# Performance work log

Measured on AMD Instinct MI355X. Metric: run time of the kernel, lower is better.

Reference implementation:

```python
import jax, jax.numpy as jnp
import numpy as np

B, M, N, C, D, H, TOPK = 32, 20000, 500000, 128, 128, 4, 100
EPS = 1e-5


def setup_inputs() -> dict:
    key = jax.random.key(0)
    ks = jax.random.split(key, 24)
    f = lambda k, s: jax.random.normal(k, s, dtype=jnp.float32) * 0.05
    inp = {
        'lhs_embedding': f(ks[0], (B, C)),
        'rhs_gnn_embedding': f(ks[1], (M, C)),
        'rhs_emb_weight': f(ks[2], (N, D)),
        'proj_W': f(ks[3], (D, C)), 'proj_b': jnp.zeros((D,), jnp.float32),
        'head_W': f(ks[4], (1, C)), 'head_b': jnp.zeros((1,), jnp.float32),
        'off_emb_W': f(ks[5], (1, D)), 'off_emb_b': jnp.zeros((1,), jnp.float32),
        'off_id_W': f(ks[6], (1, D)), 'off_id_b': jnp.zeros((1,), jnp.float32),
        'Wq': f(ks[7], (D, D)), 'bq': jnp.zeros((D,), jnp.float32),
        'Wk': f(ks[8], (D, D)), 'bk': jnp.zeros((D,), jnp.float32),
        'Wv': f(ks[9], (D, D)), 'bv': jnp.zeros((D,), jnp.float32),
        'Wo': f(ks[10], (D, D)), 'bo': jnp.zeros((D,), jnp.float32),
        'ln1_g': jnp.ones((D,), jnp.float32), 'ln1_b': jnp.zeros((D,), jnp.float32),
        'ffn_W': f(ks[11], (D, D)), 'ffn_b': jnp.zeros((D,), jnp.float32),
        'ln2_g': jnp.ones((D,), jnp.float32), 'ln2_b': jnp.zeros((D,), jnp.float32),
        'rhs_idgnn_index': jax.random.randint(ks[12], (M,), 0, N, dtype=jnp.int32),
        'lhs_idgnn_batch': jnp.sort(jax.random.randint(ks[13], (M,), 0, B, dtype=jnp.int32)),
    }
    return inp


def _ln(x, g, b):
    mu = jnp.mean(x, axis=-1, keepdims=True)
    var = jnp.mean(jnp.square(x - mu), axis=-1, keepdims=True)
    return (x - mu) * jax.lax.rsqrt(var + EPS) * g + b


def reference(lhs_embedding, rhs_gnn_embedding, rhs_emb_weight, proj_W, proj_b,
              head_W, head_b, off_emb_W, off_emb_b, off_id_W, off_id_b,
              Wq, bq, Wk, bk, Wv, bv, Wo, bo, ln1_g, ln1_b, ffn_W, ffn_b,
              ln2_g, ln2_b, rhs_idgnn_index, lhs_idgnn_batch):
    # --- embgnn logits: dense [B,N] matmul + per-row offset ---
    lhs_proj = lhs_embedding @ proj_W.T + proj_b                          # [B,D]
    embgnn_logits = lhs_proj @ rhs_emb_weight.T                           # [B,N]
    embgnn_logits = embgnn_logits + (lhs_proj @ off_emb_W[0] + off_emb_b[0])[:, None]

    # --- idgnn logits on sampled rhs nodes ---
    idgnn_logits = rhs_gnn_embedding @ head_W[0] + head_b[0]              # [M]
    idgnn_logits = idgnn_logits + jnp.sum(lhs_embedding[lhs_idgnn_batch] * rhs_gnn_embedding, axis=-1)
    idgnn_offset = lhs_proj @ off_id_W[0] + off_id_b[0]                   # [B]
    idgnn_logits = idgnn_logits + idgnn_offset[lhs_idgnn_batch]

    # scatter idgnn logits into the dense logits tensor
    embgnn_logits = embgnn_logits.at[lhs_idgnn_batch, rhs_idgnn_index].set(idgnn_logits)

    # --- final rhs embeddings: shallow table + scattered GNN embeddings ---
    copy_tensor = jnp.zeros_like(rhs_emb_weight).at[rhs_idgnn_index].set(rhs_gnn_embedding)
    final_rhs_embed = rhs_emb_weight + copy_tensor                        # [N,D]

    # --- rerank: topk -> gather -> MAB -> scatter back ---
    _, topk_index = jax.lax.top_k(embgnn_logits, TOPK)                    # [B,TOPK]
    top_embed = final_rhs_embed[topk_index]                               # [B,TOPK,D]

    dh = D // H
    q = (top_embed @ Wq.T + bq).reshape(B, TOPK, H, dh)
    k = (top_embed @ Wk.T + bk).reshape(B, TOPK, H, dh)
    v = (top_embed @ Wv.T + bv).reshape(B, TOPK, H, dh)
    att = jnp.einsum('bthd,bshd->bhts', q, k) / jnp.sqrt(jnp.float32(dh))
    att = jax.nn.softmax(att, axis=-1)
    o = jnp.einsum('bhts,bshd->bthd', att, v).reshape(B, TOPK, D) @ Wo.T + bo
    x = _ln(top_embed + o, ln1_g, ln1_b)
    x = _ln(x + jax.nn.relu(x @ ffn_W.T + ffn_b), ln2_g, ln2_b)           # tr_embed [B,TOPK,D]

    # original code passes lhs_proj[lhs_idgnn_batch] and indexes rows 0..B-1
    lhs_q = lhs_proj[lhs_idgnn_batch][:B]                                 # [B,D]
    scores = jnp.sum(lhs_q[:, None, :] * x, axis=-1)                      # [B,TOPK]
    rows = jnp.arange(B)[:, None]
    transformer_logits = jnp.full((B, N), -jnp.inf, dtype=embgnn_logits.dtype)
    transformer_logits = transformer_logits.at[rows, topk_index].set(scores)

    return embgnn_logits, transformer_logits, topk_index
```

## Files before the change

kernel.cpp:

```cpp
#include <hip/hip_runtime.h>

typedef unsigned long long u64;
typedef unsigned int u32;

#define N_NODES 500000
#define M_SAMP  20000
#define BB      32
#define DD      128
#define TOPK    100
#define NBINS   2048
#define CAP     2048
#define C4PB    3907
#define LN_EPS  1e-5f
#define NEG_BIG -1.0e30f

__device__ __forceinline__ u32 fkey(float x) {
  u32 u = __float_as_uint(x);
  u32 mask = (u32)((int)u >> 31) | 0x80000000u;
  return u ^ mask;
}

__global__ __launch_bounds__(256) void k_front(
    const float* __restrict__ lhs, const float* __restrict__ pW,
    const float* __restrict__ pb, const float* __restrict__ oeW,
    const float* __restrict__ oeb, const float* __restrict__ oiW,
    const float* __restrict__ oib, const float* __restrict__ rgnn,
    const float* __restrict__ hW, const float* __restrict__ hb,
    const int* __restrict__ ridx, const int* __restrict__ rbat,
    float* __restrict__ lhs_proj, float* __restrict__ lhs_projT,
    float* __restrict__ oe_sc, float* __restrict__ oi_sc,
    float* __restrict__ val, int* __restrict__ win,
    int* __restrict__ inv, u32* __restrict__ hist, u32* __restrict__ cand_cnt) {
  int bid = blockIdx.x, tid = threadIdx.x;
  if (bid < 32) {
    __shared__ float lrow[DD];
    __shared__ float red[DD];
    int b = bid, d = tid;
    if (d < DD) lrow[d] = lhs[b * DD + d];
    __syncthreads();
    float acc = 0.f;
    if (d < DD) {
      acc = pb[d];
      for (int c = 0; c < DD; ++c) acc += lrow[c] * pW[d * DD + c];
      lhs_proj[b * DD + d] = acc;
      lhs_projT[d * BB + b] = acc;
      red[d] = acc * oeW[d];
    }
    __syncthreads();
    for (int s = 64; s > 0; s >>= 1) { if (d < s) red[d] += red[d + s]; __syncthreads(); }
    if (d == 0) oe_sc[b] = red[0] + oeb[0];
    __syncthreads();
    if (d < DD) red[d] = acc * oiW[d];
    __syncthreads();
    for (int s = 64; s > 0; s >>= 1) { if (d < s) red[d] += red[d + s]; __syncthreads(); }
    if (d == 0) oi_sc[b] = red[0] + oib[0];
  } else if (bid < 32 + M_SAMP / 4) {
    int wid = tid >> 6, lane = tid & 63;
    int m = (bid - 32) * 4 + wid;
    if (m >= M_SAMP) return;
    int b = rbat[m], n = ridx[m];
    float2 rg = ((const float2*)(rgnn + (size_t)m * DD))[lane];
    float2 hw = ((const float2*)hW)[lane];
    float2 le = ((const float2*)(lhs + (size_t)b * DD))[lane];
    float p = rg.x * hw.x + rg.y * hw.y + rg.x * le.x + rg.y * le.y;
    for (int off = 32; off > 0; off >>= 1) p += __shfl_down(p, off);
    int w = 1;
    for (int j0 = m + 1; j0 < M_SAMP; j0 += 64) {
      int j = j0 + lane;
      bool inb = (j < M_SAMP) && (rbat[j] == b);
      bool match = inb && (ridx[j] == n);
      if (__ballot(match)) { w = 0; break; }
      if (__ballot(inb) != ~0ULL) break;
    }
    if (lane == 0) { val[m] = p + hb[0]; win[m] = w; }
  } else {
    int i = (bid - (32 + M_SAMP / 4)) * 256 + tid;
    if (i < N_NODES) inv[i] = -1;
    if (i < BB * NBINS) hist[i] = 0;
    if (i < BB) cand_cnt[i] = 0;
  }
}

__global__ __launch_bounds__(256) void k_embgnn(const float* __restrict__ rhs,
    const float* __restrict__ lhsT, const float* __restrict__ oe_sc,
    float* __restrict__ out, float* __restrict__ tr) {
  __shared__ float sT[64][DD + 4];
  int tid = threadIdx.x;
  long n0 = (long)blockIdx.x * 64;
  #pragma unroll
  for (int p = 0; p < 8; ++p) {
    int f = p * 256 + tid;
    int r = f >> 5, c4 = (f & 31) << 2;
    long n = n0 + r; if (n >= N_NODES) n = N_NODES - 1;
    float4 v = *(const float4*)(rhs + n * DD + c4);
    sT[r][c4] = v.x; sT[r][c4 + 1] = v.y; sT[r][c4 + 2] = v.z; sT[r][c4 + 3] = v.w;
  }
  __syncthreads();
  int lane = tid & 63;
  int bg = __builtin_amdgcn_readfirstlane((tid >> 6) * 8);
  float acc[8];
  #pragma unroll
  for (int j = 0; j < 8; ++j) acc[j] = 0.f;
  const float4* srow = (const float4*)&sT[lane][0];
  #pragma unroll 4
  for (int cq = 0; cq < 32; ++cq) {
    float4 rv = srow[cq];
    const float* lp = lhsT + cq * 4 * BB + bg;
    #pragma unroll
    for (int j = 0; j < 8; ++j) {
      acc[j] += lp[j] * rv.x;
      acc[j] += lp[BB + j] * rv.y;
      acc[j] += lp[2 * BB + j] * rv.z;
      acc[j] += lp[3 * BB + j] * rv.w;
    }
  }
  long n = n0 + lane;
  if (n < N_NODES) {
    #pragma unroll
    for (int j = 0; j < 8; ++j) {
      out[(long)(bg + j) * N_NODES + n] = acc[j] + oe_sc[bg + j];
      tr[(long)(bg + j) * N_NODES + n] = NEG_BIG;
    }
  }
}

__global__ void k_scatter2(const int* __restrict__ ridx, const int* __restrict__ rbat,
                           const float* __restrict__ val, const int* __restrict__ win,
                           const float* __restrict__ oi_sc,
                           int* __restrict__ inv, float* __restrict__ out) {
  int m = blockIdx.x * 256 + threadIdx.x;
  if (m < M_SAMP) {
    atomicMax(&inv[ridx[m]], m);
    if (win[m]) {
      int b = rbat[m];
      out[(long)b * N_NODES + ridx[m]] = val[m] + oi_sc[b];
    }
  }
}

__global__ void k_hist(const float* __restrict__ out, u32* __restrict__ hist) {
  __shared__ u32 hsh[NBINS];
  int tid = threadIdx.x;
  for (int i = tid; i < NBINS; i += 256) hsh[i] = 0;
  __syncthreads();
  int row = blockIdx.y;
  const float4* o4 = (const float4*)out + (long)row * (N_NODES / 4);
  int start = blockIdx.x * C4PB;
  int end = min(start + C4PB, N_NODES / 4);
  for (int i = start + tid; i < end; i += 256) {
    float4 v = o4[i];
    atomicAdd(&hsh[fkey(v.x) >> 21], 1u);
    atomicAdd(&hsh[fkey(v.y) >> 21], 1u);
    atomicAdd(&hsh[fkey(v.z) >> 21], 1u);
    atomicAdd(&hsh[fkey(v.w) >> 21], 1u);
  }
  __syncthreads();
  for (int i = tid; i < NBINS; i += 256)
    if (hsh[i]) atomicAdd(&hist[row * NBINS + i], hsh[i]);
}

__global__ void k_collect(const float* __restrict__ out, const u32* __restrict__ hist,
                          u32* __restrict__ cand_cnt, u64* __restrict__ cand) {
  __shared__ u32 part[256];
  __shared__ int s_cb;
  int tid = threadIdx.x, row = blockIdx.y;
  const u32* hrow = hist + row * NBINS;
  u32 p = 0;
  #pragma unroll
  for (int j = 0; j < 8; ++j) p += hrow[tid * 8 + j];
  part[tid] = p;
  __syncthreads();
  if (tid == 0) {
    u32 cum = 0; int g = 255, found = 0;
    for (; g > 0; --g) { cum += part[g]; if (cum >= TOPK) { found = 1; break; } }
    u32 c2 = found ? (cum - part[g]) : cum;
    int hi = found ? g * 8 + 7 : 7;
    int bin;
    for (bin = hi; bin > 0; --bin) { c2 += hrow[bin]; if (c2 >= TOPK) break; }
    s_cb = bin;
  }
  __syncthreads();
  u32 cb = (u32)s_cb;
  const float4* o4 = (const float4*)out + (long)row * (N_NODES / 4);
  int start = blockIdx.x * C4PB;
  int end = min(start + C4PB, N_NODES / 4);
  for (int i = start + tid; i < end; i += 256) {
    float4 v = o4[i];
    u32 kk[4] = { fkey(v.x), fkey(v.y), fkey(v.z), fkey(v.w) };
    #pragma unroll
    for (int j = 0; j < 4; ++j) {
      if ((kk[j] >> 21) >= cb) {
        u32 pos = atomicAdd(&cand_cnt[row], 1u);
        int idx = i * 4 + j;
        if (pos < CAP) cand[(long)row * CAP + pos] = ((u64)kk[j] << 32) | (u32)(~idx);
      }
    }
  }
}

__global__ __launch_bounds__(1024) void k_sort(const u64* __restrict__ cand,
                                               const u32* __restrict__ cand_cnt,
                                               int* __restrict__ topk_out) {
  __shared__ u64 sh[CAP];
  int row = blockIdx.x, tid = threadIdx.x;
  int cnt = min((int)cand_cnt[row], CAP);
  int NS = 128; while (NS < cnt) NS <<= 1;
  for (int i = tid; i < NS; i += 1024) sh[i] = (i < cnt) ? cand[(long)row * CAP + i] : 0ULL;
  __syncthreads();
  for (int k2 = 2; k2 <= NS; k2 <<= 1) {
    for (int j = k2 >> 1; j > 0; j >>= 1) {
      for (int i = tid; i < NS; i += 1024) {
        int ixj = i ^ j;
        if (ixj > i) {
          u64 a = sh[i], c = sh[ixj];
          bool up = ((i & k2) == 0);
          if (up ? (a < c) : (a > c)) { sh[i] = c; sh[ixj] = a; }
        }
      }
      __syncthreads();
    }
  }
  if (tid < TOPK) topk_out[row * TOPK + tid] = (int)(~(u32)sh[tid]);
}

__global__ __launch_bounds__(128) void k_gqkv(const int* __restrict__ topk,
    const int* __restrict__ inv, const float* __restrict__ rhs_emb,
    const float* __restrict__ rgnn,
    const float* __restrict__ Wq, const float* __restrict__ bq,
    const float* __restrict__ Wk, const float* __restrict__ bk,
    const float* __restrict__ Wv, const float* __restrict__ bv,
    float* __restrict__ q, float* __restrict__ k_, float* __restrict__ v_) {
  __shared__ float xr[16][DD];
  __shared__ int sn[16], sm[16];
  int tid = threadIdx.x;
  long r0 = (long)blockIdx.x * 16;
  if (tid < 16) { int n = topk[r0 + tid]; sn[tid] = n; sm[tid] = inv[n]; }
  __syncthreads();
  for (int i = tid; i < 16 * DD; i += 128) {
    int r = i >> 7, dd_ = i & 127;
    int n = sn[r], mw = sm[r];
    float v = rhs_emb[(long)n * DD + dd_];
    if (mw >= 0) v += rgnn[(long)mw * DD + dd_];
    xr[r][dd_] = v;
  }
  __syncthreads();
  float aq[16], ak[16], av[16];
  float bqv = bq[tid], bkv = bk[tid], bvv = bv[tid];
  #pragma unroll
  for (int r = 0; r < 16; ++r) { aq[r] = bqv; ak[r] = bkv; av[r] = bvv; }
  const float4* Wq4 = (const float4*)(Wq + tid * DD);
  const float4* Wk4 = (const float4*)(Wk + tid * DD);
  const float4* Wv4 = (const float4*)(Wv + tid * DD);
  #pragma unroll 4
  for (int c4 = 0; c4 < 32; ++c4) {
    float4 wq = Wq4[c4], wk = Wk4[c4], wv = Wv4[c4];
    #pragma unroll
    for (int r = 0; r < 16; ++r) {
      const float* xa = &xr[r][c4 << 2];
      float x0v = xa[0], x1v = xa[1], x2v = xa[2], x3v = xa[3];
      aq[r] += x0v * wq.x + x1v * wq.y + x2v * wq.z + x3v * wq.w;
      ak[r] += x0v * wk.x + x1v * wk.y + x2v * wk.z + x3v * wk.w;
      av[r] += x0v * wv.x + x1v * wv.y + x2v * wv.z + x3v * wv.w;
    }
  }
  #pragma unroll
  for (int r = 0; r < 16; ++r) {
    q[(r0 + r) * DD + tid] = aq[r];
    k_[(r0 + r) * DD + tid] = ak[r];
    v_[(r0 + r) * DD + tid] = av[r];
  }
}

__global__ __launch_bounds__(128) void k_att(const float* __restrict__ q,
    const float* __restrict__ k_, const float* __restrict__ v_, float* __restrict__ o) {
  __shared__ float kv[TOPK][32];
  __shared__ float att[TOPK][TOPK];
  int b = blockIdx.x >> 2, h = blockIdx.x & 3;
  int tid = threadIdx.x;
  long base = (long)b * TOPK * DD + h * 32;
  for (int i = tid; i < TOPK * 32; i += 128) {
    int t = i >> 5, d = i & 31;
    kv[t][d] = k_[base + (long)t * DD + d];
  }
  __syncthreads();
  int t = tid;
  if (t < TOPK) {
    float4 q4[8];
    const float4* qp = (const float4*)(q + base + (long)t * DD);
    #pragma unroll
    for (int i = 0; i < 8; ++i) q4[i] = qp[i];
    float qreg[32];
    #pragma unroll
    for (int i = 0; i < 8; ++i) {
      qreg[4 * i] = q4[i].x; qreg[4 * i + 1] = q4[i].y;
      qreg[4 * i + 2] = q4[i].z; qreg[4 * i + 3] = q4[i].w;
    }
    const float scale = 0.17677669529663687f;
    for (int s = 0; s < TOPK; ++s) {
      float sum = 0.f;
      #pragma unroll
      for (int d = 0; d < 32; ++d) sum += qreg[d] * kv[s][d];
      att[t][s] = sum * scale;
    }
    float mx = att[t][0];
    for (int s = 1; s < TOPK; ++s) mx = fmaxf(mx, att[t][s]);
    float sum = 0.f;
    for (int s = 0; s < TOPK; ++s) { float e = expf(att[t][s] - mx); att[t][s] = e; sum += e; }
    float inv = 1.f / sum;
    for (int s = 0; s < TOPK; ++s) att[t][s] *= inv;
  }
  __syncthreads();
  for (int i = tid; i < TOPK * 32; i += 128) {
    int tt = i >> 5, d = i & 31;
    kv[tt][d] = v_[base + (long)tt * DD + d];
  }
  __syncthreads();
  if (t < TOPK) {
    float osum[32];
    #pragma unroll
    for (int d = 0; d < 32; ++d) osum[d] = 0.f;
    for (int s = 0; s < TOPK; ++s) {
      float a = att[t][s];
      #pragma unroll
      for (int d = 0; d < 32; ++d) osum[d] += a * kv[s][d];
    }
    float4* op = (float4*)(o + base + (long)t * DD);
    #pragma unroll
    for (int i = 0; i < 8; ++i)
      op[i] = make_float4(osum[4 * i], osum[4 * i + 1], osum[4 * i + 2], osum[4 * i + 3]);
  }
}

__global__ __launch_bounds__(128) void k_xform(const float* __restrict__ ob_,
    const float* __restrict__ Wo, const float* __restrict__ bo,
    const int* __restrict__ topk, const int* __restrict__ inv,
    const float* __restrict__ rhs_emb, const float* __restrict__ rgnn,
    const float* __restrict__ g1, const float* __restrict__ be1,
    const float* __restrict__ fW, const float* __restrict__ fb,
    const float* __restrict__ g2, const float* __restrict__ be2,
    const float* __restrict__ lhs_proj, const int* __restrict__ lbat,
    float* __restrict__ tr) {
  __shared__ float sA[16][DD];
  __shared__ float sT[16][DD + 4];
  __shared__ float sMu[16], sRs[16];
  __shared__ int sn[16], sm[16];
  int tid = threadIdx.x;
  long r0 = (long)blockIdx.x * 16;
  if (tid < 16) { int n = topk[r0 + tid]; sn[tid] = n; sm[tid] = inv[n]; }
  for (int i = tid; i < 16 * DD; i += 128) sA[i >> 7][i & 127] = ob_[r0 * DD + i];
  __syncthreads();
  float vacc[16];
  #pragma unroll
  for (int r = 0; r < 16; ++r) vacc[r] = bo[tid];
  const float4* Wo4 = (const float4*)(Wo + tid * DD);
  #pragma unroll 4
  for (int c4 = 0; c4 < 32; ++c4) {
    float4 w = Wo4[c4];
    #pragma unroll
    for (int r = 0; r < 16; ++r) {
      const float* xa = &sA[r][c4 << 2];
      vacc[r] += xa[0] * w.x + xa[1] * w.y + xa[2] * w.z + xa[3] * w.w;
    }
  }
  float tval[16];
  #pragma unroll
  for (int r = 0; r < 16; ++r) {
    float x0v = rhs_emb[(long)sn[r] * DD + tid];
    if (sm[r] >= 0) x0v += rgnn[(long)sm[r] * DD + tid];
    tval[r] = vacc[r] + x0v;
    sT[r][tid] = tval[r];
  }
  __syncthreads();
  int rr = tid >> 3, sub = tid & 7;
  {
    float s = 0.f, qq = 0.f;
    const float* tp = &sT[rr][sub * 16];
    #pragma unroll
    for (int j = 0; j < 16; ++j) { float v = tp[j]; s += v; qq += v * v; }
    s += __shfl_xor(s, 1); qq += __shfl_xor(qq, 1);
    s += __shfl_xor(s, 2); qq += __shfl_xor(qq, 2);
    s += __shfl_xor(s, 4); qq += __shfl_xor(qq, 4);
    if (sub == 0) {
      float mu = s * (1.f / 128.f);
      sMu[rr] = mu;
      sRs[rr] = rsqrtf(fmaxf(qq * (1.f / 128.f) - mu * mu, 0.f) + LN_EPS);
    }
  }
  __syncthreads();
  float g1v = g1[tid], b1v = be1[tid];
  float x1v[16];
  #pragma unroll
  for (int r = 0; r < 16; ++r) {
    x1v[r] = (tval[r] - sMu[r]) * sRs[r] * g1v + b1v;
    sA[r][tid] = x1v[r];
  }
  __syncthreads();
  #pragma unroll
  for (int r = 0; r < 16; ++r) vacc[r] = fb[tid];
  const float4* fW4 = (const float4*)(fW + tid * DD);
  #pragma unroll 4
  for (int c4 = 0; c4 < 32; ++c4) {
    float4 w = fW4[c4];
    #pragma unroll
    for (int r = 0; r < 16; ++r) {
      const float* xa = &sA[r][c4 << 2];
      vacc[r] += xa[0] * w.x + xa[1] * w.y + xa[2] * w.z + xa[3] * w.w;
    }
  }
  float t2[16];
  #pragma unroll
  for (int r = 0; r < 16; ++r) { t2[r] = x1v[r] + fmaxf(vacc[r], 0.f); sT[r][tid] = t2[r]; }
  __syncthreads();
  {
    float s = 0.f, qq = 0.f;
    const float* tp = &sT[rr][sub * 16];
    #pragma unroll
    for (int j = 0; j < 16; ++j) { float v = tp[j]; s += v; qq += v * v; }
    s += __shfl_xor(s, 1); qq += __shfl_xor(qq, 1);
    s += __shfl_xor(s, 2); qq += __shfl_xor(qq, 2);
    s += __shfl_xor(s, 4); qq += __shfl_xor(qq, 4);
    if (sub == 0) {
      float mu = s * (1.f / 128.f);
      sMu[rr] = mu;
      sRs[rr] = rsqrtf(fmaxf(qq * (1.f / 128.f) - mu * mu, 0.f) + LN_EPS);
    }
  }
  __syncthreads();
  float g2v = g2[tid], b2v = be2[tid];
  #pragma unroll
  for (int r = 0; r < 16; ++r) {
    long row = r0 + r;
    int b = (int)(row / TOPK);
    float lq = lhs_proj[(long)lbat[b] * DD + tid];
    float x2 = (t2[r] - sMu[r]) * sRs[r] * g2v + b2v;
    sT[r][tid] = x2 * lq;
  }
  __syncthreads();
  {
    float s = 0.f;
    const float* tp = &sT[rr][sub * 16];
    #pragma unroll
    for (int j = 0; j < 16; ++j) s += tp[j];
    s += __shfl_xor(s, 1);
    s += __shfl_xor(s, 2);
    s += __shfl_xor(s, 4);
    if (sub == 0) {
      long row = r0 + rr;
      int b = (int)(row / TOPK);
      tr[(long)b * N_NODES + topk[row]] = s;
    }
  }
}

extern "C" void kernel_launch(void* const* d_in, const int* in_sizes, int n_in,
                              void* d_out, int out_size, void* d_ws, size_t ws_size,
                              hipStream_t stream) {
  const float* lhs_emb  = (const float*)d_in[0];
  const float* rgnn     = (const float*)d_in[1];
  const float* rhs_emb  = (const float*)d_in[2];
  const float* proj_W   = (const float*)d_in[3];
  const float* proj_b   = (const float*)d_in[4];
  const float* head_W   = (const float*)d_in[5];
  const float* head_b   = (const float*)d_in[6];
  const float* off_emb_W= (const float*)d_in[7];
  const float* off_emb_b= (const float*)d_in[8];
  const float* off_id_W = (const float*)d_in[9];
  const float* off_id_b = (const float*)d_in[10];
  const float* Wq = (const float*)d_in[11]; const float* bq = (const float*)d_in[12];
  const float* Wk = (const float*)d_in[13]; const float* bk = (const float*)d_in[14];
  const float* Wv = (const float*)d_in[15]; const float* bv = (const float*)d_in[16];
  const float* Wo = (const float*)d_in[17]; const float* bo = (const float*)d_in[18];
  const float* ln1_g = (const float*)d_in[19]; const float* ln1_b = (const float*)d_in[20];
  const float* ffn_W = (const float*)d_in[21]; const float* ffn_b = (const float*)d_in[22];
  const float* ln2_g = (const float*)d_in[23]; const float* ln2_b = (const float*)d_in[24];
  const int* ridx = (const int*)d_in[25];
  const int* rbat = (const int*)d_in[26];

  float* out_emb = (float*)d_out;
  float* out_tr  = out_emb + (long)BB * N_NODES;
  int*   out_topk = (int*)(out_emb + 2L * BB * N_NODES);

  char* w = (char*)d_ws;
  float* lhs_proj  = (float*)w; w += 16384;
  float* lhs_projT = (float*)w; w += 16384;
  float* oe_sc    = (float*)w; w += 128;
  float* oi_sc    = (float*)w; w += 128;
  float* idval    = (float*)w; w += 80000;
  int*   idwin    = (int*)w;   w += 80000;
  int*   inv      = (int*)w;   w += 2000000;
  u32*   hist     = (u32*)w;   w += BB * NBINS * 4;
  u32*   cand_cnt = (u32*)w;   w += 128;
  u64*   cand     = (u64*)w;   w += (long)BB * CAP * 8;
  float* qb = (float*)w; w += 1638400;
  float* kb = (float*)w; w += 1638400;
  float* vb = (float*)w; w += 1638400;
  float* ob = (float*)w; w += 1638400;

  const int SETUP_BLKS = (N_NODES + 255) / 256;
  k_front<<<32 + M_SAMP / 4 + SETUP_BLKS, 256, 0, stream>>>(
      lhs_emb, proj_W, proj_b, off_emb_W, off_emb_b, off_id_W, off_id_b,
      rgnn, head_W, head_b, ridx, rbat,
      lhs_proj, lhs_projT, oe_sc, oi_sc, idval, idwin, inv, hist, cand_cnt);
  k_embgnn<<<(N_NODES + 63) / 64, 256, 0, stream>>>(rhs_emb, lhs_projT, oe_sc,
                                                    out_emb, out_tr);
  k_scatter2<<<(M_SAMP + 255) / 256, 256, 0, stream>>>(ridx, rbat, idval, idwin,
                                                       oi_sc, inv, out_emb);
  k_hist<<<dim3(32, BB), 256, 0, stream>>>(out_emb, hist);
  k_collect<<<dim3(32, BB), 256, 0, stream>>>(out_emb, hist, cand_cnt, cand);
  k_sort<<<BB, 1024, 0, stream>>>(cand, cand_cnt, out_topk);

  k_gqkv<<<BB * TOPK / 16, 128, 0, stream>>>(out_topk, inv, rhs_emb, rgnn,
                                             Wq, bq, Wk, bk, Wv, bv, qb, kb, vb);
  k_att<<<BB * 4, 128, 0, stream>>>(qb, kb, vb, ob);
  k_xform<<<BB * TOPK / 16, 128, 0, stream>>>(ob, Wo, bo, out_topk, inv,
                                              rhs_emb, rgnn, ln1_g, ln1_b,
                                              ffn_W, ffn_b, ln2_g, ln2_b,
                                              lhs_proj, rbat, out_tr);
}
```

Before: 322.3 us.

## Fuse all stages into one persistent kernel with software grid barriers

Replaces the nine separate kernel launches with one persistent kernel of 384 blocks. Stages are separated by an atomic-counter grid barrier, and each stage's work is distributed with grid-stride loops. The change also splits the shared histogram into two per-bin replicas to reduce LDS atomic contention, and pairs two 16-row groups per block in the transformer stage. It aims to remove launch gaps and tail effects, but it depends on all 384 blocks being co-resident and limits parallelism in the small stages, which can cost throughput in the large matmul stage.

```diff
diff --git a/kernel.cpp b/kernel.cpp
--- a/kernel.cpp
+++ b/kernel.cpp
@@ -13,6 +13,7 @@
 #define C4PB    3907
 #define LN_EPS  1e-5f
 #define NEG_BIG -1.0e30f
+#define GRID    384
 
 __device__ __forceinline__ u32 fkey(float x) {
   u32 u = __float_as_uint(x);
@@ -20,21 +21,53 @@
   return u ^ mask;
 }
 
-__global__ __launch_bounds__(256) void k_front(
+__device__ __forceinline__ void gbar(u32* bar) {
+  __syncthreads();
+  __threadfence();
+  __syncthreads();
+  if (threadIdx.x == 0) {
+    u32 nblk = gridDim.x;
+    u32 old = atomicAdd(bar, 1u);
+    u32 target = (old / nblk + 1u) * nblk;
+    while (atomicAdd(bar, 0u) < target) __builtin_amdgcn_s_sleep(1);
+  }
+  __syncthreads();
+  __threadfence();
+  __syncthreads();
+}
+
+__global__ __launch_bounds__(256, 2) void k_mega(
     const float* __restrict__ lhs, const float* __restrict__ pW,
     const float* __restrict__ pb, const float* __restrict__ oeW,
     const float* __restrict__ oeb, const float* __restrict__ oiW,
     const float* __restrict__ oib, const float* __restrict__ rgnn,
     const float* __restrict__ hW, const float* __restrict__ hb,
     const int* __restrict__ ridx, const int* __restrict__ rbat,
-    float* __restrict__ lhs_proj, float* __restrict__ lhs_projT,
-    float* __restrict__ oe_sc, float* __restrict__ oi_sc,
-    float* __restrict__ val, int* __restrict__ win,
-    int* __restrict__ inv, u32* __restrict__ hist, u32* __restrict__ cand_cnt) {
-  int bid = blockIdx.x, tid = threadIdx.x;
-  if (bid < 32) {
-    __shared__ float lrow[DD];
-    __shared__ float red[DD];
+    const float* __restrict__ rhs_emb,
+    const float* __restrict__ Wq, const float* __restrict__ bq,
+    const float* __restrict__ Wk, const float* __restrict__ bk,
+    const float* __restrict__ Wv, const float* __restrict__ bv,
+    const float* __restrict__ Wo, const float* __restrict__ bo,
+    const float* __restrict__ g1, const float* __restrict__ be1,
+    const float* __restrict__ fW, const float* __restrict__ fb,
+    const float* __restrict__ g2, const float* __restrict__ be2,
+    float* out_emb, float* out_tr, int* out_topk,
+    float* lhs_proj, float* lhs_projT, float* oe_sc, float* oi_sc,
+    float* idval, int* idwin, int* inv, u32* hist, u32* cand_cnt, u64* cand,
+    float* qb, float* kb, float* vb, float* ob, u32* bar) {
+  __shared__ __align__(16) char smem_raw[52800];
+  __shared__ u32 s_part[256];
+  __shared__ int s_sn[32], s_sm[32], s_misc[4];
+  __shared__ float s_mu[32], s_rs[32];
+  const int bid = blockIdx.x, tid = threadIdx.x;
+  const int G = gridDim.x;
+
+  for (int i = bid * 256 + tid; i < N_NODES; i += G * 256) inv[i] = -1;
+  for (int i = bid * 256 + tid; i < BB * NBINS; i += G * 256) hist[i] = 0;
+  if (bid == 0 && tid < BB) cand_cnt[tid] = 0;
+  if (bid < BB) {
+    float* lrow = (float*)smem_raw;
+    float* red = lrow + DD;
     int b = bid, d = tid;
     if (d < DD) lrow[d] = lhs[b * DD + d];
     __syncthreads();
@@ -54,400 +87,391 @@
     __syncthreads();
     for (int s = 64; s > 0; s >>= 1) { if (d < s) red[d] += red[d + s]; __syncthreads(); }
     if (d == 0) oi_sc[b] = red[0] + oib[0];
-  } else if (bid < 32 + M_SAMP / 4) {
-    int wid = tid >> 6, lane = tid & 63;
-    int m = (bid - 32) * 4 + wid;
-    if (m >= M_SAMP) return;
-    int b = rbat[m], n = ridx[m];
-    float2 rg = ((const float2*)(rgnn + (size_t)m * DD))[lane];
-    float2 hw = ((const float2*)hW)[lane];
-    float2 le = ((const float2*)(lhs + (size_t)b * DD))[lane];
-    float p = rg.x * hw.x + rg.y * hw.y + rg.x * le.x + rg.y * le.y;
-    for (int off = 32; off > 0; off >>= 1) p += __shfl_down(p, off);
-    int w = 1;
-    for (int j0 = m + 1; j0 < M_SAMP; j0 += 64) {
-      int j = j0 + lane;
-      bool inb = (j < M_SAMP) && (rbat[j] == b);
-      bool match = inb && (ridx[j] == n);
-      if (__ballot(match)) { w = 0; break; }
-      if (__ballot(inb) != ~0ULL) break;
-    }
-    if (lane == 0) { val[m] = p + hb[0]; win[m] = w; }
-  } else {
-    int i = (bid - (32 + M_SAMP / 4)) * 256 + tid;
-    if (i < N_NODES) inv[i] = -1;
-    if (i < BB * NBINS) hist[i] = 0;
-    if (i < BB) cand_cnt[i] = 0;
-  }
-}
-
-__global__ __launch_bounds__(256) void k_embgnn(const float* __restrict__ rhs,
-    const float* __restrict__ lhsT, const float* __restrict__ oe_sc,
-    float* __restrict__ out, float* __restrict__ tr) {
-  __shared__ float sT[64][DD + 4];
-  int tid = threadIdx.x;
-  long n0 = (long)blockIdx.x * 64;
-  #pragma unroll
-  for (int p = 0; p < 8; ++p) {
-    int f = p * 256 + tid;
-    int r = f >> 5, c4 = (f & 31) << 2;
-    long n = n0 + r; if (n >= N_NODES) n = N_NODES - 1;
-    float4 v = *(const float4*)(rhs + n * DD + c4);
-    sT[r][c4] = v.x; sT[r][c4 + 1] = v.y; sT[r][c4 + 2] = v.z; sT[r][c4 + 3] = v.w;
-  }
-  __syncthreads();
-  int lane = tid & 63;
-  int bg = __builtin_amdgcn_readfirstlane((tid >> 6) * 8);
-  float acc[8];
-  #pragma unroll
-  for (int j = 0; j < 8; ++j) acc[j] = 0.f;
-  const float4* srow = (const float4*)&sT[lane][0];
-  #pragma unroll 4
-  for (int cq = 0; cq < 32; ++cq) {
-    float4 rv = srow[cq];
-    const float* lp = lhsT + cq * 4 * BB + bg;
+    __syncthreads();
+  }
+  {
+    int lane = tid & 63;
+    for (int m = bid * 4 + (tid >> 6); m < M_SAMP; m += G * 4) {
+      int b = rbat[m], n = ridx[m];
+      float2 rg = ((const float2*)(rgnn + (size_t)m * DD))[lane];
+      float2 hw = ((const float2*)hW)[lane];
+      float2 le = ((const float2*)(lhs + (size_t)b * DD))[lane];
+      float p = rg.x * hw.x + rg.y * hw.y + rg.x * le.x + rg.y * le.y;
+      for (int off = 32; off > 0; off >>= 1) p += __shfl_down(p, off);
+      int w = 1;
+      for (int j0 = m + 1; j0 < M_SAMP; j0 += 64) {
+        int j = j0 + lane;
+        bool inb = (j < M_SAMP) && (rbat[j] == b);
+        bool match = inb && (ridx[j] == n);
+        if (__ballot(match)) { w = 0; break; }
+        if (__ballot(inb) != ~0ULL) break;
+      }
+      if (lane == 0) { idval[m] = p + hb[0]; idwin[m] = w; }
+    }
+  }
+  gbar(bar);
+
+  for (int m = bid * 256 + tid; m < M_SAMP; m += G * 256)
+    atomicMax(&inv[ridx[m]], m);
+  {
+    float (*sT)[DD + 4] = (float(*)[DD + 4])smem_raw;
+    const int NT = (N_NODES + 63) / 64;
+    int lane = tid & 63;
+    int bg = __builtin_amdgcn_readfirstlane((tid >> 6) * 8);
+    for (int t = bid; t < NT; t += G) {
+      long n0 = (long)t * 64;
+      #pragma unroll
+      for (int p = 0; p < 8; ++p) {
+        int f = p * 256 + tid;
+        int r = f >> 5, c4 = (f & 31) << 2;
+        long n = n0 + r; if (n >= N_NODES) n = N_NODES - 1;
+        float4 v = *(const float4*)(rhs_emb + n * DD + c4);
+        sT[r][c4] = v.x; sT[r][c4 + 1] = v.y; sT[r][c4 + 2] = v.z; sT[r][c4 + 3] = v.w;
+      }
+      __syncthreads();
+      float acc[8];
+      #pragma unroll
+      for (int j = 0; j < 8; ++j) acc[j] = 0.f;
+      const float4* srow = (const float4*)&sT[lane][0];
+      #pragma unroll 4
+      for (int cq = 0; cq < 32; ++cq) {
+        float4 rv = srow[cq];
+        const float* lp = lhs_projT + cq * 4 * BB + bg;
+        #pragma unroll
+        for (int j = 0; j < 8; ++j) {
+          acc[j] += lp[j] * rv.x;
+          acc[j] += lp[BB + j] * rv.y;
+          acc[j] += lp[2 * BB + j] * rv.z;
+          acc[j] += lp[3 * BB + j] * rv.w;
+        }
+      }
+      long n = n0 + lane;
+      if (n < N_NODES) {
+        #pragma unroll
+        for (int j = 0; j < 8; ++j) {
+          out_emb[(long)(bg + j) * N_NODES + n] = acc[j] + oe_sc[bg + j];
+          out_tr[(long)(bg + j) * N_NODES + n] = NEG_BIG;
+        }
+      }
+      __syncthreads();
+    }
+  }
+  gbar(bar);
+
+  for (int m = bid * 256 + tid; m < M_SAMP; m += G * 256)
+    if (idwin[m]) {
+      int b = rbat[m];
+      out_emb[(long)b * N_NODES + ridx[m]] = idval[m] + oi_sc[b];
+    }
+  gbar(bar);
+
+  {
+    u32* hsh = (u32*)smem_raw;
+    for (int c = bid; c < 1024; c += G) {
+      int row = c >> 5, cx = c & 31;
+      for (int i = tid; i < NBINS * 2; i += 256) hsh[i] = 0;
+      __syncthreads();
+      const float4* o4 = (const float4*)out_emb + (long)row * (N_NODES / 4);
+      int start = cx * C4PB;
+      int end = min(start + C4PB, N_NODES / 4);
+      int rep = tid & 1;
+      for (int i = start + tid; i < end; i += 256) {
+        float4 v = o4[i];
+        atomicAdd(&hsh[(fkey(v.x) >> 21) * 2 + rep], 1u);
+        atomicAdd(&hsh[(fkey(v.y) >> 21) * 2 + rep], 1u);
+        atomicAdd(&hsh[(fkey(v.z) >> 21) * 2 + rep], 1u);
+        atomicAdd(&hsh[(fkey(v.w) >> 21) * 2 + rep], 1u);
+      }
+      __syncthreads();
+      for (int i = tid; i < NBINS; i += 256) {
+        u32 s = hsh[2 * i] + hsh[2 * i + 1];
+        if (s) atomicAdd(&hist[row * NBINS + i], s);
+      }
+      __syncthreads();
+    }
+  }
+  gbar(bar);
+
+  for (int c = bid; c < 1024; c += G) {
+    int row = c >> 5, cx = c & 31;
+    const u32* hrow = hist + row * NBINS;
+    u32 p = 0;
     #pragma unroll
-    for (int j = 0; j < 8; ++j) {
-      acc[j] += lp[j] * rv.x;
-      acc[j] += lp[BB + j] * rv.y;
-      acc[j] += lp[2 * BB + j] * rv.z;
-      acc[j] += lp[3 * BB + j] * rv.w;
-    }
-  }
-  long n = n0 + lane;
-  if (n < N_NODES) {
-    #pragma unroll
-    for (int j = 0; j < 8; ++j) {
-      out[(long)(bg + j) * N_NODES + n] = acc[j] + oe_sc[bg + j];
-      tr[(long)(bg + j) * N_NODES + n] = NEG_BIG;
-    }
-  }
-}
-
-__global__ void k_scatter2(const int* __restrict__ ridx, const int* __restrict__ rbat,
-                           const float* __restrict__ val, const int* __restrict__ win,
-                           const float* __restrict__ oi_sc,
-                           int* __restrict__ inv, float* __restrict__ out) {
-  int m = blockIdx.x * 256 + threadIdx.x;
-  if (m < M_SAMP) {
-    atomicMax(&inv[ridx[m]], m);
-    if (win[m]) {
-      int b = rbat[m];
-      out[(long)b * N_NODES + ridx[m]] = val[m] + oi_sc[b];
-    }
-  }
-}
-
-__global__ void k_hist(const float* __restrict__ out, u32* __restrict__ hist) {
-  __shared__ u32 hsh[NBINS];
-  int tid = threadIdx.x;
-  for (int i = tid; i < NBINS; i += 256) hsh[i] = 0;
-  __syncthreads();
-  int row = blockIdx.y;
-  const float4* o4 = (const float4*)out + (long)row * (N_NODES / 4);
-  int start = blockIdx.x * C4PB;
-  int end = min(start + C4PB, N_NODES / 4);
-  for (int i = start + tid; i < end; i += 256) {
-    float4 v = o4[i];
-    atomicAdd(&hsh[fkey(v.x) >> 21], 1u);
-    atomicAdd(&hsh[fkey(v.y) >> 21], 1u);
-    atomicAdd(&hsh[fkey(v.z) >> 21], 1u);
-    atomicAdd(&hsh[fkey(v.w) >> 21], 1u);
-  }
-  __syncthreads();
-  for (int i = tid; i < NBINS; i += 256)
-    if (hsh[i]) atomicAdd(&hist[row * NBINS + i], hsh[i]);
-}
-
-__global__ void k_collect(const float* __restrict__ out, const u32* __restrict__ hist,
-                          u32* __restrict__ cand_cnt, u64* __restrict__ cand) {
-  __shared__ u32 part[256];
-  __shared__ int s_cb;
-  int tid = threadIdx.x, row = blockIdx.y;
-  const u32* hrow = hist + row * NBINS;
-  u32 p = 0;
-  #pragma unroll
-  for (int j = 0; j < 8; ++j) p += hrow[tid * 8 + j];
-  part[tid] = p;
-  __syncthreads();
-  if (tid == 0) {
-    u32 cum = 0; int g = 255, found = 0;
-    for (; g > 0; --g) { cum += part[g]; if (cum >= TOPK) { found = 1; break; } }
-    u32 c2 = found ? (cum - part[g]) : cum;
-    int hi = found ? g * 8 + 7 : 7;
-    int bin;
-    for (bin = hi; bin > 0; --bin) { c2 += hrow[bin]; if (c2 >= TOPK) break; }
-    s_cb = bin;
-  }
-  __syncthreads();
-  u32 cb = (u32)s_cb;
-  const float4* o4 = (const float4*)out + (long)row * (N_NODES / 4);
-  int start = blockIdx.x * C4PB;
-  int end = min(start + C4PB, N_NODES / 4);
-  for (int i = start + tid; i < end; i += 256) {
-    float4 v = o4[i];
-    u32 kk[4] = { fkey(v.x), fkey(v.y), fkey(v.z), fkey(v.w) };
-    #pragma unroll
-    for (int j = 0; j < 4; ++j) {
-      if ((kk[j] >> 21) >= cb) {
-        u32 pos = atomicAdd(&cand_cnt[row], 1u);
-        int idx = i * 4 + j;
-        if (pos < CAP) cand[(long)row * CAP + pos] = ((u64)kk[j] << 32) | (u32)(~idx);
-      }
-    }
-  }
-}
-
-__global__ __launch_bounds__(1024) void k_sort(const u64* __restrict__ cand,
-                                               const u32* __restrict__ cand_cnt,
-                                               int* __restrict__ topk_out) {
-  __shared__ u64 sh[CAP];
-  int row = blockIdx.x, tid = threadIdx.x;
-  int cnt = min((int)cand_cnt[row], CAP);
-  int NS = 128; while (NS < cnt) NS <<= 1;
-  for (int i = tid; i < NS; i += 1024) sh[i] = (i < cnt) ? cand[(long)row * CAP + i] : 0ULL;
-  __syncthreads();
-  for (int k2 = 2; k2 <= NS; k2 <<= 1) {
-    for (int j = k2 >> 1; j > 0; j >>= 1) {
-      for (int i = tid; i < NS; i += 1024) {
-        int ixj = i ^ j;
-        if (ixj > i) {
-          u64 a = sh[i], c = sh[ixj];
-          bool up = ((i & k2) == 0);
-          if (up ? (a < c) : (a > c)) { sh[i] = c; sh[ixj] = a; }
-        }
-      }
-      __syncthreads();
-    }
-  }
-  if (tid < TOPK) topk_out[row * TOPK + tid] = (int)(~(u32)sh[tid]);
-}
-
-__global__ __launch_bounds__(128) void k_gqkv(const int* __restrict__ topk,
-    const int* __restrict__ inv, const float* __restrict__ rhs_emb,
-    const float* __restrict__ rgnn,
-    const float* __restrict__ Wq, const float* __restrict__ bq,
-    const float* __restrict__ Wk, const float* __restrict__ bk,
-    const float* __restrict__ Wv, const float* __restrict__ bv,
-    float* __restrict__ q, float* __restrict__ k_, float* __restrict__ v_) {
-  __shared__ float xr[16][DD];
-  __shared__ int sn[16], sm[16];
-  int tid = threadIdx.x;
-  long r0 = (long)blockIdx.x * 16;
-  if (tid < 16) { int n = topk[r0 + tid]; sn[tid] = n; sm[tid] = inv[n]; }
-  __syncthreads();
-  for (int i = tid; i < 16 * DD; i += 128) {
-    int r = i >> 7, dd_ = i & 127;
-    int n = sn[r], mw = sm[r];
-    float v = rhs_emb[(long)n * DD + dd_];
-    if (mw >= 0) v += rgnn[(long)mw * DD + dd_];
-    xr[r][dd_] = v;
-  }
-  __syncthreads();
-  float aq[16], ak[16], av[16];
-  float bqv = bq[tid], bkv = bk[tid], bvv = bv[tid];
-  #pragma unroll
-  for (int r = 0; r < 16; ++r) { aq[r] = bqv; ak[r] = bkv; av[r] = bvv; }
-  const float4* Wq4 = (const float4*)(Wq + tid * DD);
-  const float4* Wk4 = (const float4*)(Wk + tid * DD);
-  const float4* Wv4 = (const float4*)(Wv + tid * DD);
-  #pragma unroll 4
-  for (int c4 = 0; c4 < 32; ++c4) {
-    float4 wq = Wq4[c4], wk = Wk4[c4], wv = Wv4[c4];
-    #pragma unroll
-    for (int r = 0; r < 16; ++r) {
-      const float* xa = &xr[r][c4 << 2];
-      float x0v = xa[0], x1v = xa[1], x2v = xa[2], x3v = xa[3];
-      aq[r] += x0v * wq.x + x1v * wq.y + x2v * wq.z + x3v * wq.w;
-      ak[r] += x0v * wk.x + x1v * wk.y + x2v * wk.z + x3v * wk.w;
-      av[r] += x0v * wv.x + x1v * wv.y + x2v * wv.z + x3v * wv.w;
-    }
-  }
-  #pragma unroll
-  for (int r = 0; r < 16; ++r) {
-    q[(r0 + r) * DD + tid] = aq[r];
-    k_[(r0 + r) * DD + tid] = ak[r];
-    v_[(r0 + r) * DD + tid] = av[r];
-  }
-}
-
-__global__ __launch_bounds__(128) void k_att(const float* __restrict__ q,
-    const float* __restrict__ k_, const float* __restrict__ v_, float* __restrict__ o) {
-  __shared__ float kv[TOPK][32];
-  __shared__ float att[TOPK][TOPK];
-  int b = blockIdx.x >> 2, h = blockIdx.x & 3;
-  int tid = threadIdx.x;
-  long base = (long)b * TOPK * DD + h * 32;
-  for (int i = tid; i < TOPK * 32; i += 128) {
-    int t = i >> 5, d = i & 31;
-    kv[t][d] = k_[base + (long)t * DD + d];
-  }
-  __syncthreads();
-  int t = tid;
-  if (t < TOPK) {
-    float4 q4[8];
-    const float4* qp = (const float4*)(q + base + (long)t * DD);
-    #pragma unroll
-    for (int i = 0; i < 8; ++i) q4[i] = qp[i];
-    float qreg[32];
-    #pragma unroll
-    for (int i = 0; i < 8; ++i) {
-      qreg[4 * i] = q4[i].x; qreg[4 * i + 1] = q4[i].y;
-      qreg[4 * i + 2] = q4[i].z; qreg[4 * i + 3] = q4[i].w;
-    }
-    const float scale = 0.17677669529663687f;
-    for (int s = 0; s < TOPK; ++s) {
-      float sum = 0.f;
-      #pragma unroll
-      for (int d = 0; d < 32; ++d) sum += qreg[d] * kv[s][d];
-      att[t][s] = sum * scale;
-    }
-    float mx = att[t][0];
-    for (int s = 1; s < TOPK; ++s) mx = fmaxf(mx, att[t][s]);
-    float sum = 0.f;
-    for (int s = 0; s < TOPK; ++s) { float e = expf(att[t][s] - mx); att[t][s] = e; sum += e; }
-    float inv = 1.f / sum;
-    for (int s = 0; s < TOPK; ++s) att[t][s] *= inv;
-  }
-  __syncthreads();
-  for (int i = tid; i < TOPK * 32; i += 128) {
-    int tt = i >> 5, d = i & 31;
-    kv[tt][d] = v_[base + (long)tt * DD + d];
-  }
-  __syncthreads();
-  if (t < TOPK) {
-    float osum[32];
-    #pragma unroll
-    for (int d = 0; d < 32; ++d) osum[d] = 0.f;
-    for (int s = 0; s < TOPK; ++s) {
-      float a = att[t][s];
-      #pragma unroll
-      for (int d = 0; d < 32; ++d) osum[d] += a * kv[s][d];
-    }
-    float4* op = (float4*)(o + base + (long)t * DD);
-    #pragma unroll
-    for (int i = 0; i < 8; ++i)
-      op[i] = make_float4(osum[4 * i], osum[4 * i + 1], osum[4 * i + 2], osum[4 * i + 3]);
-  }
-}
-
-__global__ __launch_bounds__(128) void k_xform(const float* __restrict__ ob_,
-    const float* __restrict__ Wo, const float* __restrict__ bo,
-    const int* __restrict__ topk, const int* __restrict__ inv,
-    const float* __restrict__ rhs_emb, const float* __restrict__ rgnn,
-    const float* __restrict__ g1, const float* __restrict__ be1,
-    const float* __restrict__ fW, const float* __restrict__ fb,
-    const float* __restrict__ g2, const float* __restrict__ be2,
-    const float* __restrict__ lhs_proj, const int* __restrict__ lbat,
-    float* __restrict__ tr) {
-  __shared__ float sA[16][DD];
-  __shared__ float sT[16][DD + 4];
-  __shared__ float sMu[16], sRs[16];
-  __shared__ int sn[16], sm[16];
-  int tid = threadIdx.x;
-  long r0 = (long)blockIdx.x * 16;
-  if (tid < 16) { int n = topk[r0 + tid]; sn[tid] = n; sm[tid] = inv[n]; }
-  for (int i = tid; i < 16 * DD; i += 128) sA[i >> 7][i & 127] = ob_[r0 * DD + i];
-  __syncthreads();
-  float vacc[16];
-  #pragma unroll
-  for (int r = 0; r < 16; ++r) vacc[r] = bo[tid];
-  const float4* Wo4 = (const float4*)(Wo + tid * DD);
-  #pragma unroll 4
-  for (int c4 = 0; c4 < 32; ++c4) {
-    float4 w = Wo4[c4];
-    #pragma unroll
-    for (int r = 0; r < 16; ++r) {
-      const float* xa = &sA[r][c4 << 2];
-      vacc[r] += xa[0] * w.x + xa[1] * w.y + xa[2] * w.z + xa[3] * w.w;
-    }
-  }
-  float tval[16];
-  #pragma unroll
-  for (int r = 0; r < 16; ++r) {
-    float x0v = rhs_emb[(long)sn[r] * DD + tid];
-    if (sm[r] >= 0) x0v += rgnn[(long)sm[r] * DD + tid];
-    tval[r] = vacc[r] + x0v;
-    sT[r][tid] = tval[r];
-  }
-  __syncthreads();
-  int rr = tid >> 3, sub = tid & 7;
-  {
-    float s = 0.f, qq = 0.f;
-    const float* tp = &sT[rr][sub * 16];
-    #pragma unroll
-    for (int j = 0; j < 16; ++j) { float v = tp[j]; s += v; qq += v * v; }
-    s += __shfl_xor(s, 1); qq += __shfl_xor(qq, 1);
-    s += __shfl_xor(s, 2); qq += __shfl_xor(qq, 2);
-    s += __shfl_xor(s, 4); qq += __shfl_xor(qq, 4);
-    if (sub == 0) {
-      float mu = s * (1.f / 128.f);
-      sMu[rr] = mu;
-      sRs[rr] = rsqrtf(fmaxf(qq * (1.f / 128.f) - mu * mu, 0.f) + LN_EPS);
-    }
-  }
-  __syncthreads();
-  float g1v = g1[tid], b1v = be1[tid];
-  float x1v[16];
-  #pragma unroll
-  for (int r = 0; r < 16; ++r) {
-    x1v[r] = (tval[r] - sMu[r]) * sRs[r] * g1v + b1v;
-    sA[r][tid] = x1v[r];
-  }
-  __syncthreads();
-  #pragma unroll
-  for (int r = 0; r < 16; ++r) vacc[r] = fb[tid];
-  const float4* fW4 = (const float4*)(fW + tid * DD);
-  #pragma unroll 4
-  for (int c4 = 0; c4 < 32; ++c4) {
-    float4 w = fW4[c4];
-    #pragma unroll
-    for (int r = 0; r < 16; ++r) {
-      const float* xa = &sA[r][c4 << 2];
-      vacc[r] += xa[0] * w.x + xa[1] * w.y + xa[2] * w.z + xa[3] * w.w;
-    }
-  }
-  float t2[16];
-  #pragma unroll
-  for (int r = 0; r < 16; ++r) { t2[r] = x1v[r] + fmaxf(vacc[r], 0.f); sT[r][tid] = t2[r]; }
-  __syncthreads();
-  {
-    float s = 0.f, qq = 0.f;
-    const float* tp = &sT[rr][sub * 16];
-    #pragma unroll
-    for (int j = 0; j < 16; ++j) { float v = tp[j]; s += v; qq += v * v; }
-    s += __shfl_xor(s, 1); qq += __shfl_xor(qq, 1);
-    s += __shfl_xor(s, 2); qq += __shfl_xor(qq, 2);
-    s += __shfl_xor(s, 4); qq += __shfl_xor(qq, 4);
-    if (sub == 0) {
-      float mu = s * (1.f / 128.f);
-      sMu[rr] = mu;
-      sRs[rr] = rsqrtf(fmaxf(qq * (1.f / 128.f) - mu * mu, 0.f) + LN_EPS);
-    }
-  }
-  __syncthreads();
-  float g2v = g2[tid], b2v = be2[tid];
-  #pragma unroll
-  for (int r = 0; r < 16; ++r) {
-    long row = r0 + r;
-    int b = (int)(row / TOPK);
-    float lq = lhs_proj[(long)lbat[b] * DD + tid];
-    float x2 = (t2[r] - sMu[r]) * sRs[r] * g2v + b2v;
-    sT[r][tid] = x2 * lq;
-  }
-  __syncthreads();
-  {
-    float s = 0.f;
-    const float* tp = &sT[rr][sub * 16];
-    #pragma unroll
-    for (int j = 0; j < 16; ++j) s += tp[j];
-    s += __shfl_xor(s, 1);
-    s += __shfl_xor(s, 2);
-    s += __shfl_xor(s, 4);
-    if (sub == 0) {
-      long row = r0 + rr;
-      int b = (int)(row / TOPK);
-      tr[(long)b * N_NODES + topk[row]] = s;
+    for (int j = 0; j < 8; ++j) p += hrow[tid * 8 + j];
+    s_part[tid] = p;
+    __syncthreads();
+    if (tid == 0) {
+      u32 cum = 0; int g = 255, found = 0;
+      for (; g > 0; --g) { cum += s_part[g]; if (cum >= TOPK) { found = 1; break; } }
+      u32 c2 = found ? (cum - s_part[g]) : cum;
+      int hi = found ? g * 8 + 7 : 7;
+      int bin;
+      for (bin = hi; bin > 0; --bin) { c2 += hrow[bin]; if (c2 >= TOPK) break; }
+      s_misc[0] = bin;
+    }
+    __syncthreads();
+    u32 cb = (u32)s_misc[0];
+    const float4* o4 = (const float4*)out_emb + (long)row * (N_NODES / 4);
+    int start = cx * C4PB;
+    int end = min(start + C4PB, N_NODES / 4);
+    for (int i = start + tid; i < end; i += 256) {
+      float4 v = o4[i];
+      u32 kk[4] = { fkey(v.x), fkey(v.y), fkey(v.z), fkey(v.w) };
+      #pragma unroll
+      for (int j = 0; j < 4; ++j) {
+        if ((kk[j] >> 21) >= cb) {
+          u32 pos = atomicAdd(&cand_cnt[row], 1u);
+          if (pos < CAP) cand[(long)row * CAP + pos] = ((u64)kk[j] << 32) | (u32)(~(i * 4 + j));
+        }
+      }
+    }
+    __syncthreads();
+  }
+  gbar(bar);
+
+  {
+    u64* sh = (u64*)smem_raw;
+    for (int row = bid; row < BB; row += G) {
+      int cnt = min((int)cand_cnt[row], CAP);
+      int NS = 128; while (NS < cnt) NS <<= 1;
+      for (int i = tid; i < NS; i += 256) sh[i] = (i < cnt) ? cand[(long)row * CAP + i] : 0ULL;
+      __syncthreads();
+      for (int k2 = 2; k2 <= NS; k2 <<= 1) {
+        for (int j = k2 >> 1; j > 0; j >>= 1) {
+          for (int i = tid; i < NS; i += 256) {
+            int ixj = i ^ j;
+            if (ixj > i) {
+              u64 a = sh[i], cc = sh[ixj];
+              bool up = ((i & k2) == 0);
+              if (up ? (a < cc) : (a > cc)) { sh[i] = cc; sh[ixj] = a; }
+            }
+          }
+          __syncthreads();
+        }
+      }
+      if (tid < TOPK) out_topk[row * TOPK + tid] = (int)(~(u32)sh[tid]);
+      __syncthreads();
+    }
+  }
+  gbar(bar);
+
+  {
+    float* xr = (float*)smem_raw;
+    int half = tid >> 7, t = tid & 127;
+    for (int gp = bid; gp < (BB * TOPK) / 32; gp += G) {
+      int g = gp * 2 + half;
+      long r0 = (long)g * 16;
+      if (t < 16) { int n = out_topk[r0 + t]; s_sn[half * 16 + t] = n; s_sm[half * 16 + t] = inv[n]; }
+      __syncthreads();
+      float* xrh = xr + half * 16 * DD;
+      for (int i = t; i < 16 * DD; i += 128) {
+        int r = i >> 7, dd_ = i & 127;
+        int n = s_sn[half * 16 + r], mw = s_sm[half * 16 + r];
+        float v = rhs_emb[(long)n * DD + dd_];
+        if (mw >= 0) v += rgnn[(long)mw * DD + dd_];
+        xrh[i] = v;
+      }
+      __syncthreads();
+      float aq[16], ak[16], av[16];
+      float bqv = bq[t], bkv = bk[t], bvv = bv[t];
+      #pragma unroll
+      for (int r = 0; r < 16; ++r) { aq[r] = bqv; ak[r] = bkv; av[r] = bvv; }
+      const float4* Wq4 = (const float4*)(Wq + t * DD);
+      const float4* Wk4 = (const float4*)(Wk + t * DD);
+      const float4* Wv4 = (const float4*)(Wv + t * DD);
+      #pragma unroll 4
+      for (int c4 = 0; c4 < 32; ++c4) {
+        float4 wq = Wq4[c4], wk = Wk4[c4], wv = Wv4[c4];
+        #pragma unroll
+        for (int r = 0; r < 16; ++r) {
+          const float* xa = &xrh[r * DD + (c4 << 2)];
+          float x0v = xa[0], x1v = xa[1], x2v = xa[2], x3v = xa[3];
+          aq[r] += x0v * wq.x + x1v * wq.y + x2v * wq.z + x3v * wq.w;
+          ak[r] += x0v * wk.x + x1v * wk.y + x2v * wk.z + x3v * wk.w;
+          av[r] += x0v * wv.x + x1v * wv.y + x2v * wv.z + x3v * wv.w;
+        }
+      }
+      #pragma unroll
+      for (int r = 0; r < 16; ++r) {
+        qb[(r0 + r) * DD + t] = aq[r];
+        kb[(r0 + r) * DD + t] = ak[r];
+        vb[(r0 + r) * DD + t] = av[r];
+      }
+      __syncthreads();
+    }
+  }
+  gbar(bar);
+
+  {
+    float* kv = (float*)smem_raw;
+    float* aw = (float*)(smem_raw + 12800);
+    for (int pair = bid; pair < BB * 4; pair += G) {
+      int b = pair >> 2, h = pair & 3;
+      long base = (long)b * TOPK * DD + h * 32;
+      for (int i = tid; i < TOPK * 32; i += 256)
+        kv[i] = kb[base + (long)(i >> 5) * DD + (i & 31)];
+      __syncthreads();
+      int t = tid;
+      if (t < TOPK) {
+        float qreg[32];
+        const float4* qp = (const float4*)(qb + base + (long)t * DD);
+        #pragma unroll
+        for (int i = 0; i < 8; ++i) {
+          float4 q4 = qp[i];
+          qreg[4 * i] = q4.x; qreg[4 * i + 1] = q4.y; qreg[4 * i + 2] = q4.z; qreg[4 * i + 3] = q4.w;
+        }
+        const float scale = 0.17677669529663687f;
+        for (int s = 0; s < TOPK; ++s) {
+          float sum = 0.f;
+          #pragma unroll
+          for (int d = 0; d < 32; ++d) sum += qreg[d] * kv[s * 32 + d];
+          aw[t * TOPK + s] = sum * scale;
+        }
+        float mx = aw[t * TOPK];
+        for (int s = 1; s < TOPK; ++s) mx = fmaxf(mx, aw[t * TOPK + s]);
+        float sum = 0.f;
+        for (int s = 0; s < TOPK; ++s) { float e = expf(aw[t * TOPK + s] - mx); aw[t * TOPK + s] = e; sum += e; }
+        float is = 1.f / sum;
+        for (int s = 0; s < TOPK; ++s) aw[t * TOPK + s] *= is;
+      }
+      __syncthreads();
+      for (int i = tid; i < TOPK * 32; i += 256)
+        kv[i] = vb[base + (long)(i >> 5) * DD + (i & 31)];
+      __syncthreads();
+      if (t < TOPK) {
+        float osum[32];
+        #pragma unroll
+        for (int d = 0; d < 32; ++d) osum[d] = 0.f;
+        for (int s = 0; s < TOPK; ++s) {
+          float a = aw[t * TOPK + s];
+          #pragma unroll
+          for (int d = 0; d < 32; ++d) osum[d] += a * kv[s * 32 + d];
+        }
+        float4* op = (float4*)(ob + base + (long)t * DD);
+        #pragma unroll
+        for (int i = 0; i < 8; ++i)
+          op[i] = make_float4(osum[4 * i], osum[4 * i + 1], osum[4 * i + 2], osum[4 * i + 3]);
+      }
+      __syncthreads();
+    }
+  }
+  gbar(bar);
+
+  {
+    float* sA = (float*)smem_raw;
+    float* sTT = (float*)(smem_raw + 16384);
+    int half = tid >> 7, t = tid & 127;
+    int rr = t >> 3, sub = t & 7;
+    int mh = half * 16;
+    for (int gp = bid; gp < (BB * TOPK) / 32; gp += G) {
+      int g = gp * 2 + half;
+      long r0 = (long)g * 16;
+      if (t < 16) { int n = out_topk[r0 + t]; s_sn[mh + t] = n; s_sm[mh + t] = inv[n]; }
+      float* sAh = sA + half * 16 * DD;
+      float* sTh = sTT + half * 16 * 132;
+      for (int i = t; i < 16 * DD; i += 128) sAh[i] = ob[r0 * DD + i];
+      __syncthreads();
+      float vacc[16];
+      #pragma unroll
+      for (int r = 0; r < 16; ++r) vacc[r] = bo[t];
+      const float4* Wo4 = (const float4*)(Wo + t * DD);
+      #pragma unroll 4
+      for (int c4 = 0; c4 < 32; ++c4) {
+        float4 w = Wo4[c4];
+        #pragma unroll
+        for (int r = 0; r < 16; ++r) {
+          const float* xa = &sAh[r * DD + (c4 << 2)];
+          vacc[r] += xa[0] * w.x + xa[1] * w.y + xa[2] * w.z + xa[3] * w.w;
+        }
+      }
+      float tval[16];
+      #pragma unroll
+      for (int r = 0; r < 16; ++r) {
+        float x0v = rhs_emb[(long)s_sn[mh + r] * DD + t];
+        if (s_sm[mh + r] >= 0) x0v += rgnn[(long)s_sm[mh + r] * DD + t];
+        tval[r] = vacc[r] + x0v;
+        sTh[r * 132 + t] = tval[r];
+      }
+      __syncthreads();
+      {
+        float s = 0.f, qq = 0.f;
+        const float* tp = &sTh[rr * 132 + sub * 16];
+        #pragma unroll
+        for (int j = 0; j < 16; ++j) { float v = tp[j]; s += v; qq += v * v; }
+        s += __shfl_xor(s, 1); qq += __shfl_xor(qq, 1);
+        s += __shfl_xor(s, 2); qq += __shfl_xor(qq, 2);
+        s += __shfl_xor(s, 4); qq += __shfl_xor(qq, 4);
+        if (sub == 0) {
+          float mu = s * (1.f / 128.f);
+          s_mu[mh + rr] = mu;
+          s_rs[mh + rr] = rsqrtf(fmaxf(qq * (1.f / 128.f) - mu * mu, 0.f) + LN_EPS);
+        }
+      }
+      __syncthreads();
+      float g1v = g1[t], b1v = be1[t];
+      float x1v[16];
+      #pragma unroll
+      for (int r = 0; r < 16; ++r) {
+        x1v[r] = (tval[r] - s_mu[mh + r]) * s_rs[mh + r] * g1v + b1v;
+        sAh[r * DD + t] = x1v[r];
+      }
+      __syncthreads();
+      #pragma unroll
+      for (int r = 0; r < 16; ++r) vacc[r] = fb[t];
+      const float4* fW4 = (const float4*)(fW + t * DD);
+      #pragma unroll 4
+      for (int c4 = 0; c4 < 32; ++c4) {
+        float4 w = fW4[c4];
+        #pragma unroll
+        for (int r = 0; r < 16; ++r) {
+          const float* xa = &sAh[r * DD + (c4 << 2)];
+          vacc[r] += xa[0] * w.x + xa[1] * w.y + xa[2] * w.z + xa[3] * w.w;
+        }
+      }
+      float t2[16];
+      #pragma unroll
+      for (int r = 0; r < 16; ++r) { t2[r] = x1v[r] + fmaxf(vacc[r], 0.f); sTh[r * 132 + t] = t2[r]; }
+      __syncthreads();
+      {
+        float s = 0.f, qq = 0.f;
+        const float* tp = &sTh[rr * 132 + sub * 16];
+        #pragma unroll
+        for (int j = 0; j < 16; ++j) { float v = tp[j]; s += v; qq += v * v; }
+        s += __shfl_xor(s, 1); qq += __shfl_xor(qq, 1);
+        s += __shfl_xor(s, 2); qq += __shfl_xor(qq, 2);
+        s += __shfl_xor(s, 4); qq += __shfl_xor(qq, 4);
+        if (sub == 0) {
+          float mu = s * (1.f / 128.f);
+          s_mu[mh + rr] = mu;
+          s_rs[mh + rr] = rsqrtf(fmaxf(qq * (1.f / 128.f) - mu * mu, 0.f) + LN_EPS);
+        }
+      }
+      __syncthreads();
+      float g2v = g2[t], b2v = be2[t];
+      #pragma unroll
+      for (int r = 0; r < 16; ++r) {
+        long row = r0 + r;
+        int b = (int)(row / TOPK);
+        float lq = lhs_proj[(long)rbat[b] * DD + t];
+        float x2 = (t2[r] - s_mu[mh + r]) * s_rs[mh + r] * g2v + b2v;
+        sTh[r * 132 + t] = x2 * lq;
+      }
+      __syncthreads();
+      {
+        float s = 0.f;
+        const float* tp = &sTh[rr * 132 + sub * 16];
+        #pragma unroll
+        for (int j = 0; j < 16; ++j) s += tp[j];
+        s += __shfl_xor(s, 1);
+        s += __shfl_xor(s, 2);
+        s += __shfl_xor(s, 4);
+        if (sub == 0) {
+          long row = r0 + rr;
+          int b = (int)(row / TOPK);
+          out_tr[(long)b * N_NODES + out_topk[row]] = s;
+        }
+      }
+      __syncthreads();
     }
   }
 }
@@ -495,25 +519,14 @@
   float* kb = (float*)w; w += 1638400;
   float* vb = (float*)w; w += 1638400;
   float* ob = (float*)w; w += 1638400;
-
-  const int SETUP_BLKS = (N_NODES + 255) / 256;
-  k_front<<<32 + M_SAMP / 4 + SETUP_BLKS, 256, 0, stream>>>(
+  u32*   bar = (u32*)w; w += 64;
+
+  hipMemsetAsync(bar, 0, 64, stream);
+  k_mega<<<GRID, 256, 0, stream>>>(
       lhs_emb, proj_W, proj_b, off_emb_W, off_emb_b, off_id_W, off_id_b,
-      rgnn, head_W, head_b, ridx, rbat,
-      lhs_proj, lhs_projT, oe_sc, oi_sc, idval, idwin, inv, hist, cand_cnt);
-  k_embgnn<<<(N_NODES + 63) / 64, 256, 0, stream>>>(rhs_emb, lhs_projT, oe_sc,
-                                                    out_emb, out_tr);
-  k_scatter2<<<(M_SAMP + 255) / 256, 256, 0, stream>>>(ridx, rbat, idval, idwin,
-                                                       oi_sc, inv, out_emb);
-  k_hist<<<dim3(32, BB), 256, 0, stream>>>(out_emb, hist);
-  k_collect<<<dim3(32, BB), 256, 0, stream>>>(out_emb, hist, cand_cnt, cand);
-  k_sort<<<BB, 1024, 0, stream>>>(cand, cand_cnt, out_topk);
-
-  k_gqkv<<<BB * TOPK / 16, 128, 0, stream>>>(out_topk, inv, rhs_emb, rgnn,
-                                             Wq, bq, Wk, bk, Wv, bv, qb, kb, vb);
-  k_att<<<BB * 4, 128, 0, stream>>>(qb, kb, vb, ob);
-  k_xform<<<BB * TOPK / 16, 128, 0, stream>>>(ob, Wo, bo, out_topk, inv,
-                                              rhs_emb, rgnn, ln1_g, ln1_b,
-                                              ffn_W, ffn_b, ln2_g, ln2_b,
-                                              lhs_proj, rbat, out_tr);
+      rgnn, head_W, head_b, ridx, rbat, rhs_emb,
+      Wq, bq, Wk, bk, Wv, bv, Wo, bo, ln1_g, ln1_b, ffn_W, ffn_b, ln2_g, ln2_b,
+      out_emb, out_tr, out_topk,
+      lhs_proj, lhs_projT, oe_sc, oi_sc, idval, idwin, inv, hist, cand_cnt, cand,
+      qb, kb, vb, ob, bar);
 }
```

Result: slower. 1.253 ms (+288.6%).
